# Kernel tuning notes

Hardware: AMD Instinct MI355X
Metric: run time of the kernel (lower is better)

## Reference

```python
import jax, jax.numpy as jnp
import numpy as np
from jax import lax

N_NODES = 10000
N_EDGES = 160000
F_NODE = 128
C_GCN = 64
S_SEQ = 32
T_SEQ = 96
H_LSTM = 128


def setup_inputs() -> dict:
    key = jax.random.key(0)
    ks = jax.random.split(key, 20)
    inp = {
        "sequences": jax.random.normal(ks[0], (N_NODES, T_SEQ, S_SEQ), jnp.float32),
        "edge_index": jax.random.randint(ks[1], (2, N_EDGES), 0, N_NODES, jnp.int64),
        "edge_attr": jax.random.uniform(ks[2], (N_EDGES, 1), jnp.float32),
        "node_features": jax.random.normal(ks[3], (N_NODES, F_NODE), jnp.float32),
        "node_indices": jax.random.randint(ks[4], (N_NODES,), 0, N_NODES, jnp.int64),
    }
    s_g = 1.0 / np.sqrt(F_NODE)
    inp["gcn_w"] = jax.random.uniform(ks[5], (F_NODE, C_GCN), jnp.float32, -s_g, s_g)
    inp["gcn_b"] = jnp.zeros((C_GCN,), jnp.float32)
    in0 = S_SEQ + C_GCN
    s_l = 1.0 / np.sqrt(H_LSTM)
    inp["w_ih0"] = jax.random.uniform(ks[6], (4 * H_LSTM, in0), jnp.float32, -s_l, s_l)
    inp["w_hh0"] = jax.random.uniform(ks[7], (4 * H_LSTM, H_LSTM), jnp.float32, -s_l, s_l)
    inp["b_ih0"] = jax.random.uniform(ks[8], (4 * H_LSTM,), jnp.float32, -s_l, s_l)
    inp["b_hh0"] = jax.random.uniform(ks[9], (4 * H_LSTM,), jnp.float32, -s_l, s_l)
    inp["w_ih1"] = jax.random.uniform(ks[10], (4 * H_LSTM, H_LSTM), jnp.float32, -s_l, s_l)
    inp["w_hh1"] = jax.random.uniform(ks[11], (4 * H_LSTM, H_LSTM), jnp.float32, -s_l, s_l)
    inp["b_ih1"] = jax.random.uniform(ks[12], (4 * H_LSTM,), jnp.float32, -s_l, s_l)
    inp["b_hh1"] = jax.random.uniform(ks[13], (4 * H_LSTM,), jnp.float32, -s_l, s_l)
    s_f = 1.0 / np.sqrt(H_LSTM)
    inp["fc_w"] = jax.random.uniform(ks[14], (1, H_LSTM), jnp.float32, -s_f, s_f)
    inp["fc_b"] = jnp.zeros((1,), jnp.float32)
    return inp


def gcn_conv(x, edge_index, w, b):
    """PyG GCNConv: out = D^{-1/2} (A + I) D^{-1/2} X W + b."""
    n = x.shape[0]
    xw = x @ w  # [N, C]
    loop = jnp.arange(n, dtype=edge_index.dtype)
    row = jnp.concatenate([edge_index[0], loop])  # source j
    col = jnp.concatenate([edge_index[1], loop])  # target i
    deg = jax.ops.segment_sum(jnp.ones_like(col, dtype=xw.dtype), col, num_segments=n)
    dinv = jnp.where(deg > 0, lax.rsqrt(deg), 0.0)
    norm = dinv[row] * dinv[col]  # [E+N]
    msg = xw[row] * norm[:, None]  # gather + scale
    out = jax.ops.segment_sum(msg, col, num_segments=n)  # scatter-add
    return out + b


def lstm_layer(x, w_ih, w_hh, b_ih, b_hh):
    """batch_first LSTM layer; torch gate order i,f,g,o. x: [N,T,I] -> [N,T,H]."""
    n, t, _ = x.shape
    h_dim = w_hh.shape[1]
    xg = jnp.einsum("nti,gi->ntg", x, w_ih) + b_ih + b_hh  # [N,T,4H]

    def step(carry, xt):
        h, c = carry
        g = xt + h @ w_hh.T
        i, f, gg, o = jnp.split(g, 4, axis=-1)
        c = jax.nn.sigmoid(f) * c + jax.nn.sigmoid(i) * jnp.tanh(gg)
        h = jax.nn.sigmoid(o) * jnp.tanh(c)
        return (h, c), h

    h0 = jnp.zeros((n, h_dim), x.dtype)
    _, hs = lax.scan(step, (h0, h0), jnp.swapaxes(xg, 0, 1))
    return jnp.swapaxes(hs, 0, 1)


def reference(sequences, edge_index, edge_attr, node_features, node_indices,
              gcn_w, gcn_b, w_ih0, w_hh0, b_ih0, b_hh0,
              w_ih1, w_hh1, b_ih1, b_hh1, fc_w, fc_b):
    # GCN over the static graph (dropout = identity in eval mode)
    gcn_out = gcn_conv(node_features, edge_index, gcn_w, gcn_b)  # [N, C]
    t = sequences.shape[1]
    gcn_rep = jnp.broadcast_to(gcn_out[:, None, :], (gcn_out.shape[0], t, gcn_out.shape[1]))
    combined = jnp.concatenate([sequences, gcn_rep], axis=-1)  # [N, T, S+C]
    h = lstm_layer(combined, w_ih0, w_hh0, b_ih0, b_hh0)
    h = lstm_layer(h, w_ih1, w_hh1, b_ih1, b_hh1)
    last = h[:, -1, :]  # [N, H]
    return last @ fc_w.T + fc_b  # [N, 1]
```

## Files before the change

### kernel.cpp

```cpp
#include <hip/hip_runtime.h>
#include <hip/hip_bf16.h>

typedef _Float16 half8 __attribute__((ext_vector_type(8)));
typedef float floatx4 __attribute__((ext_vector_type(4)));
typedef float floatx2 __attribute__((ext_vector_type(2)));

#define N_NODES 10000
#define F_NODE  128
#define C_GCN   64
#define N_EDGES 160000
#define T_SEQ   96
#define S_SEQ   32
#define HID     128
#define M_BLK   40
#define MT      3
#define SEQ_STRIDE 104
#define H_STRIDE   136
#define WAVE_STREAM 61440

__device__ __forceinline__ float fast_rcp(float x) { return __builtin_amdgcn_rcpf(x); }
__device__ __forceinline__ float sigm_f(float x) {
    return fast_rcp(1.0f + __expf(-x));
}
__device__ __forceinline__ float tanh_f(float x) {
    return 2.0f * fast_rcp(1.0f + __expf(-2.0f * x)) - 1.0f;
}

__global__ void k_gcn_xw(const float* __restrict__ nf, const float* __restrict__ w,
                         float* __restrict__ xw) {
    int tid = blockIdx.x * 256 + threadIdx.x;
    int n = tid >> 6, c = tid & 63;
    if (n >= N_NODES) return;
    float s = 0.f;
    #pragma unroll 8
    for (int k = 0; k < F_NODE; ++k) s = fmaf(nf[n * F_NODE + k], w[k * C_GCN + c], s);
    xw[n * C_GCN + c] = s;
}

__global__ void k_deg_init(float* __restrict__ deg) {
    int i = blockIdx.x * 256 + threadIdx.x;
    if (i < N_NODES) deg[i] = 1.0f;
}

__global__ void k_deg_count(const int* __restrict__ ei, float* __restrict__ deg) {
    int e = blockIdx.x * 256 + threadIdx.x;
    if (e < N_EDGES) atomicAdd(&deg[ei[N_EDGES + e]], 1.0f);
}

__global__ void k_dinv(const float* __restrict__ deg, float* __restrict__ dinv) {
    int i = blockIdx.x * 256 + threadIdx.x;
    if (i < N_NODES) dinv[i] = rsqrtf(deg[i]);
}

__global__ void k_gcn_self(const float* __restrict__ xw, const float* __restrict__ dinv,
                           const float* __restrict__ gb, float* __restrict__ gout) {
    int tid = blockIdx.x * 256 + threadIdx.x;
    int n = tid >> 6, c = tid & 63;
    if (n >= N_NODES) return;
    float di = dinv[n];
    gout[tid] = xw[tid] * di * di + gb[c];
}

__global__ void k_gcn_scatter(const int* __restrict__ ei, const float* __restrict__ xw,
                              const float* __restrict__ dinv, float* __restrict__ gout) {
    int e = blockIdx.x * 4 + (threadIdx.x >> 6);
    int c = threadIdx.x & 63;
    if (e >= N_EDGES) return;
    int r  = ei[e];
    int cl = ei[N_EDGES + e];
    float nm = dinv[r] * dinv[cl];
    atomicAdd(&gout[cl * C_GCN + c], xw[r * C_GCN + c] * nm);
}

__global__ void k_pack(const float* __restrict__ w_ih0, const float* __restrict__ w_hh0,
                       const float* __restrict__ w_ih1, const float* __restrict__ w_hh1,
                       half8* __restrict__ pP) {
    int tid = blockIdx.x * 256 + threadIdx.x;
    if (tid >= 8 * 15 * 4 * 64) return;
    int lane = tid & 63;
    int g    = (tid >> 6) & 3;
    int s    = (tid >> 8) % 15;
    int w    = tid / 3840;
    const float* src; int kt, K;
    if (s < 3)       { src = w_ih0; kt = s;      K = 96;  }
    else if (s < 7)  { src = w_hh0; kt = s - 3;  K = 128; }
    else if (s < 11) { src = w_ih1; kt = s - 7;  K = 128; }
    else             { src = w_hh1; kt = s - 11; K = 128; }
    int row = g * 128 + w * 16 + (lane & 15);
    int k0  = kt * 32 + (lane >> 4) * 8;
    half8 v;
    #pragma unroll
    for (int j = 0; j < 8; ++j) v[j] = (_Float16)src[row * K + k0 + j];
    pP[tid] = v;
}

__global__ void k_bsum(const float* __restrict__ bi0, const float* __restrict__ bh0,
                       const float* __restrict__ bi1, const float* __restrict__ bh1,
                       float* __restrict__ bs) {
    int i = blockIdx.x * 256 + threadIdx.x;
    if (i < 512)       bs[i] = bi0[i] + bh0[i];
    else if (i < 1024) bs[i] = bi1[i - 512] + bh1[i - 512];
}


__device__ __forceinline__ void async_copy16(const void* g, void* l) {
    __builtin_amdgcn_global_load_lds(
        (const __attribute__((address_space(1))) unsigned int*)g,
        (__attribute__((address_space(3))) unsigned int*)l, 16, 0, 0);
}

__device__ __forceinline__ void dma_slot(const char* __restrict__ src, int lane, _Float16* slot) {
    #pragma unroll
    for (int g = 0; g < 4; ++g)
        async_copy16((const void*)(src + g * 1024 + lane * 16), (void*)(slot + g * 512));
}

#define VMWAIT8() asm volatile("s_waitcnt vmcnt(8)" ::: "memory")

#define BARRIER_NOVM() do {                                   \
    asm volatile("s_waitcnt lgkmcnt(0)" ::: "memory");        \
    __builtin_amdgcn_s_barrier();                             \
    asm volatile("" ::: "memory");                            \
} while (0)

__device__ __forceinline__ void mfma_kt(floatx4 acc[4][MT], const _Float16* slot, int lane,
                                        const _Float16* A, int strideA, int koff,
                                        int l15, int quad) {
    half8 bg[4], a[MT];
    #pragma unroll
    for (int g = 0; g < 4; ++g) bg[g] = *(const half8*)(slot + g * 512 + lane * 8);
    #pragma unroll
    for (int mt = 0; mt < MT; ++mt)
        a[mt] = *(const half8*)(A + (mt * 16 + l15) * strideA + koff + quad * 8);
    #pragma unroll
    for (int g = 0; g < 4; ++g)
        #pragma unroll
        for (int mt = 0; mt < MT; ++mt)
            acc[g][mt] = __builtin_amdgcn_mfma_f32_16x16x32_f16(a[mt], bg[g], acc[g][mt], 0, 0, 0);
}

__device__ __forceinline__ void epilogue(floatx4 acc[4][MT],
                                         float c[MT][4], _Float16* Hnext,
                                         int quad, int ch) {
    #pragma unroll
    for (int mt = 0; mt < MT; ++mt) {
        #pragma unroll
        for (int r = 0; r < 4; ++r) {
            float gi = acc[0][mt][r];
            float gf = acc[1][mt][r];
            float gg = acc[2][mt][r];
            float go = acc[3][mt][r];
            float cn = sigm_f(gf) * c[mt][r] + sigm_f(gi) * tanh_f(gg);
            c[mt][r] = cn;
            float h = sigm_f(go) * tanh_f(cn);
            Hnext[(mt * 16 + quad * 4 + r) * H_STRIDE + ch] = (_Float16)h;
        }
    }
}

__global__ __launch_bounds__(512, 2) void k_lstm(
    const float* __restrict__ seq, const float* __restrict__ gcn,
    const char* __restrict__ pW, const float* __restrict__ bsum,
    const float* __restrict__ fcw, const float* __restrict__ fcb,
    float* __restrict__ out) {

    __shared__ __align__(16) _Float16 sSeq[48 * SEQ_STRIDE];
    __shared__ __align__(16) _Float16 sH0[2][48 * H_STRIDE];
    __shared__ __align__(16) _Float16 sH1[2][48 * H_STRIDE];
    __shared__ __align__(16) _Float16 sWa[8][2048];
    __shared__ __align__(16) _Float16 sWb[8][2048];
    __shared__ __align__(16) _Float16 sWc[8][2048];

    const int tid  = threadIdx.x;
    const int wid  = tid >> 6;
    const int lane = tid & 63;
    const int l15  = lane & 15;
    const int quad = lane >> 4;
    const int node0 = blockIdx.x * M_BLK;
    const int ch = wid * 16 + l15;

    const char* pWw = pW + wid * WAVE_STREAM;

#define DMA(S, RING)                  dma_slot(pWw + (S) * 4096, lane, &RING[wid][0])
#define USE(RING, Aptr, stride, koff) mfma_kt(acc, &RING[wid][0], lane, (Aptr), (stride), (koff), l15, quad)

    DMA(0, sWa);
    DMA(1, sWb);

    for (int i = tid; i < 48 * SEQ_STRIDE; i += 512) sSeq[i] = (_Float16)0.f;
    for (int i = tid; i < 48 * H_STRIDE; i += 512) {
        sH0[0][i] = (_Float16)0.f; sH0[1][i] = (_Float16)0.f;
        sH1[0][i] = (_Float16)0.f; sH1[1][i] = (_Float16)0.f;
    }

    float bias0[4], bias1[4];
    #pragma unroll
    for (int g = 0; g < 4; ++g) {
        bias0[g] = bsum[g * 128 + ch];
        bias1[g] = bsum[512 + g * 128 + ch];
    }

    float c0[MT][4] = {{0}}, c1[MT][4] = {{0}};

    __syncthreads();

    for (int i = tid; i < M_BLK * (C_GCN / 2); i += 512) {
        int r = i >> 5, cp = (i & 31) * 2;
        floatx2 v = *(const floatx2*)(gcn + (size_t)(node0 + r) * C_GCN + cp);
        sSeq[r * SEQ_STRIDE + S_SEQ + cp]     = (_Float16)v.x;
        sSeq[r * SEQ_STRIDE + S_SEQ + cp + 1] = (_Float16)v.y;
    }
    {
        int r = tid >> 4, cp = (tid & 15) * 2;
        if (tid < M_BLK * 16) {
            floatx2 v = *(const floatx2*)(seq + ((size_t)(node0 + r) * T_SEQ) * S_SEQ + cp);
            sSeq[r * SEQ_STRIDE + cp]     = (_Float16)v.x;
            sSeq[r * SEQ_STRIDE + cp + 1] = (_Float16)v.y;
        }
    }
    __syncthreads();

    floatx4 acc[4][MT];
    const int pr = tid >> 4, pc = (tid & 15) * 2;

    for (int t = 0; t < T_SEQ; ++t) {
        const int cur = t & 1, nxt = cur ^ 1;
        const _Float16* h0c = &sH0[cur][0];
        _Float16*       h0n = &sH0[nxt][0];
        const _Float16* h1c = &sH1[cur][0];
        _Float16*       h1n = &sH1[nxt][0];

        floatx2 pf0 = {0.f, 0.f}, pf1 = {0.f, 0.f};
        if (t + 1 < T_SEQ) {
            pf0 = *(const floatx2*)(seq + ((size_t)(node0 + pr) * T_SEQ + (t + 1)) * S_SEQ + pc);
            if (tid < 128) {
                int r1 = (512 + tid) >> 4, c1r = ((512 + tid) & 15) * 2;
                pf1 = *(const floatx2*)(seq + ((size_t)(node0 + r1) * T_SEQ + (t + 1)) * S_SEQ + c1r);
            }
        }

        #pragma unroll
        for (int g = 0; g < 4; ++g) {
            floatx4 bv = {bias0[g], bias0[g], bias0[g], bias0[g]};
            #pragma unroll
            for (int mt = 0; mt < MT; ++mt) acc[g][mt] = bv;
        }
        DMA(2, sWc);  VMWAIT8();  USE(sWa, sSeq, SEQ_STRIDE, 0);
        DMA(3, sWa);  VMWAIT8();  USE(sWb, sSeq, SEQ_STRIDE, 32);
        DMA(4, sWb);  VMWAIT8();  USE(sWc, sSeq, SEQ_STRIDE, 64);
        DMA(5, sWc);  VMWAIT8();  USE(sWa, h0c, H_STRIDE, 0);
        DMA(6, sWa);  VMWAIT8();  USE(sWb, h0c, H_STRIDE, 32);
        DMA(7, sWb);  VMWAIT8();  USE(sWc, h0c, H_STRIDE, 64);
        DMA(8, sWc);  VMWAIT8();  USE(sWa, h0c, H_STRIDE, 96);
        epilogue(acc, c0, h0n, quad, ch);
        BARRIER_NOVM();

        #pragma unroll
        for (int g = 0; g < 4; ++g) {
            floatx4 bv = {bias1[g], bias1[g], bias1[g], bias1[g]};
            #pragma unroll
            for (int mt = 0; mt < MT; ++mt) acc[g][mt] = bv;
        }
        DMA(9,  sWa); VMWAIT8();  USE(sWb, h0n, H_STRIDE, 0);
        DMA(10, sWb); VMWAIT8();  USE(sWc, h0n, H_STRIDE, 32);
        DMA(11, sWc); VMWAIT8();  USE(sWa, h0n, H_STRIDE, 64);
        DMA(12, sWa); VMWAIT8();  USE(sWb, h0n, H_STRIDE, 96);
        DMA(13, sWb); VMWAIT8();  USE(sWc, h1c, H_STRIDE, 0);
        DMA(14, sWc); VMWAIT8();  USE(sWa, h1c, H_STRIDE, 32);
        DMA(0,  sWa); VMWAIT8();  USE(sWb, h1c, H_STRIDE, 64);
        DMA(1,  sWb); VMWAIT8();  USE(sWc, h1c, H_STRIDE, 96);

        if (t + 1 < T_SEQ) {
            sSeq[pr * SEQ_STRIDE + pc]     = (_Float16)pf0.x;
            sSeq[pr * SEQ_STRIDE + pc + 1] = (_Float16)pf0.y;
            if (tid < 128) {
                int r1 = (512 + tid) >> 4, c1r = ((512 + tid) & 15) * 2;
                sSeq[r1 * SEQ_STRIDE + c1r]     = (_Float16)pf1.x;
                sSeq[r1 * SEQ_STRIDE + c1r + 1] = (_Float16)pf1.y;
            }
        }
        epilogue(acc, c1, h1n, quad, ch);
        BARRIER_NOVM();
    }

#undef DMA
#undef USE

    asm volatile("s_waitcnt vmcnt(0)" ::: "memory");

    if (tid < M_BLK) {
        const _Float16* h1 = &sH1[0][tid * H_STRIDE];
        float s = fcb[0];
        #pragma unroll 16
        for (int k = 0; k < HID; ++k) s = fmaf((float)h1[k], fcw[k], s);
        out[node0 + tid] = s;
    }
}

extern "C" void kernel_launch(void* const* d_in, const int* in_sizes, int n_in,
                              void* d_out, int out_size, void* d_ws, size_t ws_size,
                              hipStream_t stream) {
    const float* seq   = (const float*)d_in[0];
    const int*   ei    = (const int*)d_in[1];
    const float* nf    = (const float*)d_in[3];
    const float* gcn_w = (const float*)d_in[5];
    const float* gcn_b = (const float*)d_in[6];
    const float* w_ih0 = (const float*)d_in[7];
    const float* w_hh0 = (const float*)d_in[8];
    const float* b_ih0 = (const float*)d_in[9];
    const float* b_hh0 = (const float*)d_in[10];
    const float* w_ih1 = (const float*)d_in[11];
    const float* w_hh1 = (const float*)d_in[12];
    const float* b_ih1 = (const float*)d_in[13];
    const float* b_hh1 = (const float*)d_in[14];
    const float* fc_w  = (const float*)d_in[15];
    const float* fc_b  = (const float*)d_in[16];
    float* out = (float*)d_out;

    char* ws = (char*)d_ws;
    float* xw   = (float*)(ws);
    float* gout = (float*)(ws + 2621440);
    float* deg  = (float*)(ws + 5242880);
    float* dinv = (float*)(ws + 5283840);
    float* bsum = (float*)(ws + 5324800);
    char*  pP   = (char*)(ws + 5328896);

    k_gcn_xw     <<<2500,  256, 0, stream>>>(nf, gcn_w, xw);
    k_deg_init   <<<40,    256, 0, stream>>>(deg);
    k_deg_count  <<<625,   256, 0, stream>>>(ei, deg);
    k_dinv       <<<40,    256, 0, stream>>>(deg, dinv);
    k_gcn_self   <<<2500,  256, 0, stream>>>(xw, dinv, gcn_b, gout);
    k_gcn_scatter<<<40000, 256, 0, stream>>>(ei, xw, dinv, gout);

    k_pack<<<120, 256, 0, stream>>>(w_ih0, w_hh0, w_ih1, w_hh1, (half8*)pP);
    k_bsum<<<4,   256, 0, stream>>>(b_ih0, b_hh0, b_ih1, b_hh1, bsum);

    k_lstm<<<250, 512, 0, stream>>>(seq, gout, pP, bsum, fc_w, fc_b, out);
}
```

Measured before the change: 1.284 ms.

## Split LSTM layers across wave groups with a one-step wavefront pipeline

In the old kernel every wave ran layer 0 and then layer 1 in sequence, with a barrier between them. Now waves 0-3 run only layer 0 and waves 4-7 run only layer 1, and layer 1 trails by one timestep, so the two layers' work overlaps inside each step. Each wave now covers 32 gate channels instead of 16, and the weight packing and sequence prefetch are rearranged to match, with an extra drain iteration after the loop for layer 1. The aim is to remove the serialization between the layers and the idle time at the mid-step barrier. In exchange the two groups carry unequal work (14 versus 16 weight slots), each thread holds twice as many accumulators, and the timing of the H buffer double-buffering becomes more delicate.

```diff
diff --git a/kernel.cpp b/kernel.cpp
--- a/kernel.cpp
+++ b/kernel.cpp
@@ -16,7 +16,8 @@
 #define MT      3
 #define SEQ_STRIDE 104
 #define H_STRIDE   136
-#define WAVE_STREAM 61440
+#define L0_STREAM 57344
+#define L1_BASE   229376
 
 __device__ __forceinline__ float fast_rcp(float x) { return __builtin_amdgcn_rcpf(x); }
 __device__ __forceinline__ float sigm_f(float x) {
@@ -74,24 +75,33 @@
 
 __global__ void k_pack(const float* __restrict__ w_ih0, const float* __restrict__ w_hh0,
                        const float* __restrict__ w_ih1, const float* __restrict__ w_hh1,
-                       half8* __restrict__ pP) {
+                       char* __restrict__ pP) {
     int tid = blockIdx.x * 256 + threadIdx.x;
-    if (tid >= 8 * 15 * 4 * 64) return;
+    if (tid >= 120 * 256) return;
     int lane = tid & 63;
     int g    = (tid >> 6) & 3;
-    int s    = (tid >> 8) % 15;
-    int w    = tid / 3840;
-    const float* src; int kt, K;
-    if (s < 3)       { src = w_ih0; kt = s;      K = 96;  }
-    else if (s < 7)  { src = w_hh0; kt = s - 3;  K = 128; }
-    else if (s < 11) { src = w_ih1; kt = s - 7;  K = 128; }
-    else             { src = w_hh1; kt = s - 11; K = 128; }
-    int row = g * 128 + w * 16 + (lane & 15);
+    int gs   = tid >> 8;
+    int w, s, ch0, K, kt, n;
+    const float* src;
+    size_t base;
+    if (gs < 56) {
+        w = gs / 14; s = gs % 14; ch0 = w * 32;
+        base = (size_t)w * L0_STREAM;
+        if (s < 6) { src = w_ih0; kt = s >> 1;       n = s & 1;       K = 96;  }
+        else       { src = w_hh0; kt = (s - 6) >> 1; n = (s - 6) & 1; K = 128; }
+    } else {
+        int g2 = gs - 56;
+        w = g2 / 16; s = g2 % 16; ch0 = w * 32;
+        base = (size_t)L1_BASE + (size_t)w * 65536;
+        if (s < 8) { src = w_ih1; kt = s >> 1;       n = s & 1;       K = 128; }
+        else       { src = w_hh1; kt = (s - 8) >> 1; n = (s - 8) & 1; K = 128; }
+    }
+    int row = g * 128 + ch0 + n * 16 + (lane & 15);
     int k0  = kt * 32 + (lane >> 4) * 8;
     half8 v;
     #pragma unroll
     for (int j = 0; j < 8; ++j) v[j] = (_Float16)src[row * K + k0 + j];
-    pP[tid] = v;
+    *(half8*)(pP + base + (size_t)s * 4096 + g * 1024 + lane * 16) = v;
 }
 
 __global__ void k_bsum(const float* __restrict__ bi0, const float* __restrict__ bh0,
@@ -115,7 +125,7 @@
         async_copy16((const void*)(src + g * 1024 + lane * 16), (void*)(slot + g * 512));
 }
 
-#define VMWAIT8() asm volatile("s_waitcnt vmcnt(8)" ::: "memory")
+#define VMW(N) asm volatile("s_waitcnt vmcnt(" #N ")" ::: "memory")
 
 #define BARRIER_NOVM() do {                                   \
     asm volatile("s_waitcnt lgkmcnt(0)" ::: "memory");        \
@@ -123,39 +133,53 @@
     asm volatile("" ::: "memory");                            \
 } while (0)
 
-__device__ __forceinline__ void mfma_kt(floatx4 acc[4][MT], const _Float16* slot, int lane,
-                                        const _Float16* A, int strideA, int koff,
-                                        int l15, int quad) {
-    half8 bg[4], a[MT];
+#define LDB(BASE) {                                                         \
+    _Pragma("unroll")                                                       \
+    for (int g = 0; g < 4; ++g) bg[g] = *(const half8*)((BASE) + g * 512 + lane * 8); }
+
+#define MM(N) {                                                             \
+    _Pragma("unroll")                                                       \
+    for (int g = 0; g < 4; ++g)                                             \
+        _Pragma("unroll")                                                   \
+        for (int mt = 0; mt < MT; ++mt)                                     \
+            acc[g][N][mt] = __builtin_amdgcn_mfma_f32_16x16x32_f16(a[mt], bg[g], acc[g][N][mt], 0, 0, 0); }
+
+#define SLOT_N0(BASE, APTR, ASTR, KOFF) { LDB(BASE);                        \
+    _Pragma("unroll")                                                       \
+    for (int mt = 0; mt < MT; ++mt)                                         \
+        a[mt] = *(const half8*)((APTR) + (mt * 16 + l15) * (ASTR) + (KOFF) + quad * 8); \
+    MM(0); }
+#define SLOT_N1(BASE) { LDB(BASE); MM(1); }
+
+#define DMA2(S, BASE) dma_slot(pWw + (S) * 4096, lane, (BASE))
+
+#define ACCINIT() {                                                         \
+    _Pragma("unroll")                                                       \
+    for (int g = 0; g < 4; ++g)                                             \
+        _Pragma("unroll")                                                   \
+        for (int n = 0; n < 2; ++n) {                                       \
+            floatx4 bv = {bias[g][n], bias[g][n], bias[g][n], bias[g][n]};  \
+            _Pragma("unroll")                                               \
+            for (int mt = 0; mt < MT; ++mt) acc[g][n][mt] = bv;             \
+        } }
+
+__device__ __forceinline__ void epilogue2(floatx4 acc[4][2][MT], float cst[2][MT][4],
+                                          _Float16* H, int quad, int ch0, int l15) {
     #pragma unroll
-    for (int g = 0; g < 4; ++g) bg[g] = *(const half8*)(slot + g * 512 + lane * 8);
-    #pragma unroll
-    for (int mt = 0; mt < MT; ++mt)
-        a[mt] = *(const half8*)(A + (mt * 16 + l15) * strideA + koff + quad * 8);
-    #pragma unroll
-    for (int g = 0; g < 4; ++g)
+    for (int n = 0; n < 2; ++n)
         #pragma unroll
         for (int mt = 0; mt < MT; ++mt)
-            acc[g][mt] = __builtin_amdgcn_mfma_f32_16x16x32_f16(a[mt], bg[g], acc[g][mt], 0, 0, 0);
-}
-
-__device__ __forceinline__ void epilogue(floatx4 acc[4][MT],
-                                         float c[MT][4], _Float16* Hnext,
-                                         int quad, int ch) {
-    #pragma unroll
-    for (int mt = 0; mt < MT; ++mt) {
-        #pragma unroll
-        for (int r = 0; r < 4; ++r) {
-            float gi = acc[0][mt][r];
-            float gf = acc[1][mt][r];
-            float gg = acc[2][mt][r];
-            float go = acc[3][mt][r];
-            float cn = sigm_f(gf) * c[mt][r] + sigm_f(gi) * tanh_f(gg);
-            c[mt][r] = cn;
-            float h = sigm_f(go) * tanh_f(cn);
-            Hnext[(mt * 16 + quad * 4 + r) * H_STRIDE + ch] = (_Float16)h;
-        }
-    }
+            #pragma unroll
+            for (int r = 0; r < 4; ++r) {
+                float gi = acc[0][n][mt][r];
+                float gf = acc[1][n][mt][r];
+                float gg = acc[2][n][mt][r];
+                float go = acc[3][n][mt][r];
+                float cn = sigm_f(gf) * cst[n][mt][r] + sigm_f(gi) * tanh_f(gg);
+                cst[n][mt][r] = cn;
+                H[(mt * 16 + quad * 4 + r) * H_STRIDE + ch0 + n * 16 + l15] =
+                    (_Float16)(sigm_f(go) * tanh_f(cn));
+            }
 }
 
 __global__ __launch_bounds__(512, 2) void k_lstm(
@@ -177,15 +201,15 @@
     const int l15  = lane & 15;
     const int quad = lane >> 4;
     const int node0 = blockIdx.x * M_BLK;
-    const int ch = wid * 16 + l15;
-
-    const char* pWw = pW + wid * WAVE_STREAM;
-
-#define DMA(S, RING)                  dma_slot(pWw + (S) * 4096, lane, &RING[wid][0])
-#define USE(RING, Aptr, stride, koff) mfma_kt(acc, &RING[wid][0], lane, (Aptr), (stride), (koff), l15, quad)
-
-    DMA(0, sWa);
-    DMA(1, sWb);
+    const bool isL0 = (wid < 4);
+    const int ch0 = (wid & 3) * 32;
+
+    _Float16* const rb0 = &sWa[wid][0];
+    _Float16* const rb1 = &sWb[wid][0];
+    _Float16* const rb2 = &sWc[wid][0];
+
+    const char* pWw = pW + (isL0 ? (size_t)wid * L0_STREAM
+                                 : (size_t)L1_BASE + (size_t)(wid - 4) * 65536);
 
     for (int i = tid; i < 48 * SEQ_STRIDE; i += 512) sSeq[i] = (_Float16)0.f;
     for (int i = tid; i < 48 * H_STRIDE; i += 512) {
@@ -193,14 +217,17 @@
         sH1[0][i] = (_Float16)0.f; sH1[1][i] = (_Float16)0.f;
     }
 
-    float bias0[4], bias1[4];
-    #pragma unroll
-    for (int g = 0; g < 4; ++g) {
-        bias0[g] = bsum[g * 128 + ch];
-        bias1[g] = bsum[512 + g * 128 + ch];
-    }
-
-    float c0[MT][4] = {{0}}, c1[MT][4] = {{0}};
+    float bias[4][2];
+    {
+        int off = isL0 ? 0 : 512;
+        #pragma unroll
+        for (int g = 0; g < 4; ++g)
+            #pragma unroll
+            for (int n = 0; n < 2; ++n)
+                bias[g][n] = bsum[off + g * 128 + ch0 + n * 16 + l15];
+    }
+
+    float cst[2][MT][4] = {{{0}}};
 
     __syncthreads();
 
@@ -212,84 +239,126 @@
     }
     {
         int r = tid >> 4, cp = (tid & 15) * 2;
-        if (tid < M_BLK * 16) {
-            floatx2 v = *(const floatx2*)(seq + ((size_t)(node0 + r) * T_SEQ) * S_SEQ + cp);
-            sSeq[r * SEQ_STRIDE + cp]     = (_Float16)v.x;
-            sSeq[r * SEQ_STRIDE + cp + 1] = (_Float16)v.y;
+        floatx2 v = *(const floatx2*)(seq + ((size_t)(node0 + r) * T_SEQ) * S_SEQ + cp);
+        sSeq[r * SEQ_STRIDE + cp]     = (_Float16)v.x;
+        sSeq[r * SEQ_STRIDE + cp + 1] = (_Float16)v.y;
+        if (tid < 128) {
+            int r2 = (512 + tid) >> 4;
+            floatx2 w = *(const floatx2*)(seq + ((size_t)(node0 + r2) * T_SEQ) * S_SEQ + cp);
+            sSeq[r2 * SEQ_STRIDE + cp]     = (_Float16)w.x;
+            sSeq[r2 * SEQ_STRIDE + cp + 1] = (_Float16)w.y;
         }
     }
     __syncthreads();
 
-    floatx4 acc[4][MT];
-    const int pr = tid >> 4, pc = (tid & 15) * 2;
-
-    for (int t = 0; t < T_SEQ; ++t) {
-        const int cur = t & 1, nxt = cur ^ 1;
-        const _Float16* h0c = &sH0[cur][0];
-        _Float16*       h0n = &sH0[nxt][0];
-        const _Float16* h1c = &sH1[cur][0];
-        _Float16*       h1n = &sH1[nxt][0];
-
-        floatx2 pf0 = {0.f, 0.f}, pf1 = {0.f, 0.f};
-        if (t + 1 < T_SEQ) {
-            pf0 = *(const floatx2*)(seq + ((size_t)(node0 + pr) * T_SEQ + (t + 1)) * S_SEQ + pc);
-            if (tid < 128) {
-                int r1 = (512 + tid) >> 4, c1r = ((512 + tid) & 15) * 2;
-                pf1 = *(const floatx2*)(seq + ((size_t)(node0 + r1) * T_SEQ + (t + 1)) * S_SEQ + c1r);
-            }
+    const int tid2 = tid & 255;
+    const int pr0 = tid2 >> 4, pcp = (tid2 & 15) * 2;
+    floatx2 pfa = {0.f, 0.f}, pfb = {0.f, 0.f}, pfc = {0.f, 0.f};
+
+#define PF_ISSUE(T) do { if ((T) <= 95) {                                               \
+        pfa = *(const floatx2*)(seq + ((size_t)(node0 + pr0)      * T_SEQ + (T)) * S_SEQ + pcp); \
+        pfb = *(const floatx2*)(seq + ((size_t)(node0 + pr0 + 16) * T_SEQ + (T)) * S_SEQ + pcp); \
+        if (tid2 < 128)                                                                 \
+        pfc = *(const floatx2*)(seq + ((size_t)(node0 + pr0 + 32) * T_SEQ + (T)) * S_SEQ + pcp); \
+    } } while (0)
+
+#define COMMIT_SEQ() do { if (u < 95) {                                                 \
+        sSeq[pr0 * SEQ_STRIDE + pcp]            = (_Float16)pfa.x;                      \
+        sSeq[pr0 * SEQ_STRIDE + pcp + 1]        = (_Float16)pfa.y;                      \
+        sSeq[(pr0 + 16) * SEQ_STRIDE + pcp]     = (_Float16)pfb.x;                      \
+        sSeq[(pr0 + 16) * SEQ_STRIDE + pcp + 1] = (_Float16)pfb.y;                      \
+        if (tid2 < 128) {                                                               \
+            sSeq[(pr0 + 32) * SEQ_STRIDE + pcp]     = (_Float16)pfc.x;                  \
+            sSeq[(pr0 + 32) * SEQ_STRIDE + pcp + 1] = (_Float16)pfc.y;                  \
+        } } } while (0)
+
+    if (!isL0) PF_ISSUE(1);
+    DMA2(0, rb0);
+    DMA2(1, rb1);
+
+    floatx4 acc[4][2][MT];
+    half8 a[MT], bg[4];
+
+    for (int u = 0; u < 96; ++u) {
+        const int wp = u & 1, rp = wp ^ 1;
+
+        if (isL0) {
+            const _Float16* h0r = &sH0[rp][0];
+            _Float16*       h0w = &sH0[wp][0];
+            ACCINIT();
+            DMA2(2, rb2);  VMW(8); SLOT_N0(rb0, sSeq, SEQ_STRIDE, 0);
+            DMA2(3, rb0);  VMW(8); SLOT_N1(rb1);
+            DMA2(4, rb1);  VMW(8); SLOT_N0(rb2, sSeq, SEQ_STRIDE, 32);
+            DMA2(5, rb2);  VMW(8); SLOT_N1(rb0);
+            DMA2(6, rb0);  VMW(8); SLOT_N0(rb1, sSeq, SEQ_STRIDE, 64);
+            DMA2(7, rb1);  VMW(8); SLOT_N1(rb2);
+            BARRIER_NOVM();
+            DMA2(8, rb2);  VMW(8); SLOT_N0(rb0, h0r, H_STRIDE, 0);
+            DMA2(9, rb0);  VMW(8); SLOT_N1(rb1);
+            DMA2(10, rb1); VMW(8); SLOT_N0(rb2, h0r, H_STRIDE, 32);
+            DMA2(11, rb2); VMW(8); SLOT_N1(rb0);
+            DMA2(12, rb0); VMW(8); SLOT_N0(rb1, h0r, H_STRIDE, 64);
+            DMA2(13, rb1); VMW(8); SLOT_N1(rb2);
+            VMW(4); SLOT_N0(rb0, h0r, H_STRIDE, 96); DMA2(0, rb0);
+            VMW(4); SLOT_N1(rb1);                    DMA2(1, rb1);
+            epilogue2(acc, cst, h0w, quad, ch0, l15);
+            BARRIER_NOVM();
+        } else {
+            const _Float16* h0r = &sH0[rp][0];
+            const _Float16* h1r = &sH1[wp][0];
+            _Float16*       h1w = &sH1[rp][0];
+            ACCINIT();
+            DMA2(2, rb2);  VMW(4); SLOT_N0(rb0, h0r, H_STRIDE, 0);
+            DMA2(3, rb0);  VMW(8); SLOT_N1(rb1);
+            DMA2(4, rb1);  VMW(8); SLOT_N0(rb2, h0r, H_STRIDE, 32);
+            DMA2(5, rb2);  VMW(8); SLOT_N1(rb0);
+            DMA2(6, rb0);  VMW(8); SLOT_N0(rb1, h0r, H_STRIDE, 64);
+            DMA2(7, rb1);  VMW(8); SLOT_N1(rb2);
+            DMA2(8, rb2);  VMW(8); SLOT_N0(rb0, h0r, H_STRIDE, 96);
+            DMA2(9, rb0);  VMW(8); SLOT_N1(rb1);
+            BARRIER_NOVM();
+            COMMIT_SEQ();
+            DMA2(10, rb1); VMW(8); SLOT_N0(rb2, h1r, H_STRIDE, 0);
+            DMA2(11, rb2); VMW(8); SLOT_N1(rb0);
+            DMA2(12, rb0); VMW(8); SLOT_N0(rb1, h1r, H_STRIDE, 32);
+            DMA2(13, rb1); VMW(8); SLOT_N1(rb2);
+            DMA2(14, rb2); VMW(8); SLOT_N0(rb0, h1r, H_STRIDE, 64);
+            DMA2(15, rb0); VMW(8); SLOT_N1(rb1);
+            DMA2(1, rb1);  VMW(8); SLOT_N0(rb2, h1r, H_STRIDE, 96);
+            VMW(4); SLOT_N1(rb0); PF_ISSUE(u + 2); DMA2(0, rb0);
+            if (u) epilogue2(acc, cst, h1w, quad, ch0, l15);
+            BARRIER_NOVM();
         }
-
-        #pragma unroll
-        for (int g = 0; g < 4; ++g) {
-            floatx4 bv = {bias0[g], bias0[g], bias0[g], bias0[g]};
-            #pragma unroll
-            for (int mt = 0; mt < MT; ++mt) acc[g][mt] = bv;
-        }
-        DMA(2, sWc);  VMWAIT8();  USE(sWa, sSeq, SEQ_STRIDE, 0);
-        DMA(3, sWa);  VMWAIT8();  USE(sWb, sSeq, SEQ_STRIDE, 32);
-        DMA(4, sWb);  VMWAIT8();  USE(sWc, sSeq, SEQ_STRIDE, 64);
-        DMA(5, sWc);  VMWAIT8();  USE(sWa, h0c, H_STRIDE, 0);
-        DMA(6, sWa);  VMWAIT8();  USE(sWb, h0c, H_STRIDE, 32);
-        DMA(7, sWb);  VMWAIT8();  USE(sWc, h0c, H_STRIDE, 64);
-        DMA(8, sWc);  VMWAIT8();  USE(sWa, h0c, H_STRIDE, 96);
-        epilogue(acc, c0, h0n, quad, ch);
-        BARRIER_NOVM();
-
-        #pragma unroll
-        for (int g = 0; g < 4; ++g) {
-            floatx4 bv = {bias1[g], bias1[g], bias1[g], bias1[g]};
-            #pragma unroll
-            for (int mt = 0; mt < MT; ++mt) acc[g][mt] = bv;
-        }
-        DMA(9,  sWa); VMWAIT8();  USE(sWb, h0n, H_STRIDE, 0);
-        DMA(10, sWb); VMWAIT8();  USE(sWc, h0n, H_STRIDE, 32);
-        DMA(11, sWc); VMWAIT8();  USE(sWa, h0n, H_STRIDE, 64);
-        DMA(12, sWa); VMWAIT8();  USE(sWb, h0n, H_STRIDE, 96);
-        DMA(13, sWb); VMWAIT8();  USE(sWc, h1c, H_STRIDE, 0);
-        DMA(14, sWc); VMWAIT8();  USE(sWa, h1c, H_STRIDE, 32);
-        DMA(0,  sWa); VMWAIT8();  USE(sWb, h1c, H_STRIDE, 64);
-        DMA(1,  sWb); VMWAIT8();  USE(sWc, h1c, H_STRIDE, 96);
-
-        if (t + 1 < T_SEQ) {
-            sSeq[pr * SEQ_STRIDE + pc]     = (_Float16)pf0.x;
-            sSeq[pr * SEQ_STRIDE + pc + 1] = (_Float16)pf0.y;
-            if (tid < 128) {
-                int r1 = (512 + tid) >> 4, c1r = ((512 + tid) & 15) * 2;
-                sSeq[r1 * SEQ_STRIDE + c1r]     = (_Float16)pf1.x;
-                sSeq[r1 * SEQ_STRIDE + c1r + 1] = (_Float16)pf1.y;
-            }
-        }
-        epilogue(acc, c1, h1n, quad, ch);
-        BARRIER_NOVM();
-    }
-
-#undef DMA
-#undef USE
-
+    }
+
+    if (!isL0) {
+        const _Float16* h0r = &sH0[1][0];
+        const _Float16* h1r = &sH1[0][0];
+        _Float16*       h1w = &sH1[1][0];
+        ACCINIT();
+        DMA2(2, rb2);  VMW(4); SLOT_N0(rb0, h0r, H_STRIDE, 0);
+        DMA2(3, rb0);  VMW(8); SLOT_N1(rb1);
+        DMA2(4, rb1);  VMW(8); SLOT_N0(rb2, h0r, H_STRIDE, 32);
+        DMA2(5, rb2);  VMW(8); SLOT_N1(rb0);
+        DMA2(6, rb0);  VMW(8); SLOT_N0(rb1, h0r, H_STRIDE, 64);
+        DMA2(7, rb1);  VMW(8); SLOT_N1(rb2);
+        DMA2(8, rb2);  VMW(8); SLOT_N0(rb0, h0r, H_STRIDE, 96);
+        DMA2(9, rb0);  VMW(8); SLOT_N1(rb1);
+        DMA2(10, rb1); VMW(8); SLOT_N0(rb2, h1r, H_STRIDE, 0);
+        DMA2(11, rb2); VMW(8); SLOT_N1(rb0);
+        DMA2(12, rb0); VMW(8); SLOT_N0(rb1, h1r, H_STRIDE, 32);
+        DMA2(13, rb1); VMW(8); SLOT_N1(rb2);
+        DMA2(14, rb2); VMW(8); SLOT_N0(rb0, h1r, H_STRIDE, 64);
+        DMA2(15, rb0); VMW(8); SLOT_N1(rb1);
+        VMW(4); SLOT_N0(rb2, h1r, H_STRIDE, 96);
+        VMW(0); SLOT_N1(rb0);
+        epilogue2(acc, cst, h1w, quad, ch0, l15);
+    }
     asm volatile("s_waitcnt vmcnt(0)" ::: "memory");
+    __syncthreads();
 
     if (tid < M_BLK) {
-        const _Float16* h1 = &sH1[0][tid * H_STRIDE];
+        const _Float16* h1 = &sH1[1][tid * H_STRIDE];
         float s = fcb[0];
         #pragma unroll 16
         for (int k = 0; k < HID; ++k) s = fmaf((float)h1[k], fcw[k], s);
@@ -332,7 +401,7 @@
     k_gcn_self   <<<2500,  256, 0, stream>>>(xw, dinv, gcn_b, gout);
     k_gcn_scatter<<<40000, 256, 0, stream>>>(ei, xw, dinv, gout);
 
-    k_pack<<<120, 256, 0, stream>>>(w_ih0, w_hh0, w_ih1, w_hh1, (half8*)pP);
+    k_pack<<<120, 256, 0, stream>>>(w_ih0, w_hh0, w_ih1, w_hh1, pP);
     k_bsum<<<4,   256, 0, stream>>>(b_ih0, b_hh0, b_ih1, b_hh1, bsum);
 
     k_lstm<<<250, 512, 0, stream>>>(seq, gout, pP, bsum, fc_w, fc_b, out);
```

New measurement: 2.609 ms. 103% more time.

## Software-pipeline LDS operand reads one k-tile ahead of MFMAs in LSTM loop

Applied to the files above, without the earlier changes.

Replaces the per-k-tile load-then-MFMA helper with double-buffered register fragments (aX/aY, bX/bY), so the LDS reads for the next k-tile are issued before the MFMAs of the current one. The vmcnt wait is tightened to match the new three-slot prefetch distance. The sequence prefetch loads become unconditional, using a clamped timestep and a fixed row mapping, which removes branches. This raises register pressure and depends on the hand-written wait counts being right for the async weight DMA ring.

```diff
diff --git a/kernel.cpp b/kernel.cpp
--- a/kernel.cpp
+++ b/kernel.cpp
@@ -115,7 +115,7 @@
         async_copy16((const void*)(src + g * 1024 + lane * 16), (void*)(slot + g * 512));
 }
 
-#define VMWAIT8() asm volatile("s_waitcnt vmcnt(8)" ::: "memory")
+#define VMW(N) asm volatile("s_waitcnt vmcnt(" #N ")" ::: "memory")
 
 #define BARRIER_NOVM() do {                                   \
     asm volatile("s_waitcnt lgkmcnt(0)" ::: "memory");        \
@@ -123,21 +123,29 @@
     asm volatile("" ::: "memory");                            \
 } while (0)
 
-__device__ __forceinline__ void mfma_kt(floatx4 acc[4][MT], const _Float16* slot, int lane,
-                                        const _Float16* A, int strideA, int koff,
-                                        int l15, int quad) {
-    half8 bg[4], a[MT];
-    #pragma unroll
-    for (int g = 0; g < 4; ++g) bg[g] = *(const half8*)(slot + g * 512 + lane * 8);
-    #pragma unroll
-    for (int mt = 0; mt < MT; ++mt)
-        a[mt] = *(const half8*)(A + (mt * 16 + l15) * strideA + koff + quad * 8);
-    #pragma unroll
-    for (int g = 0; g < 4; ++g)
-        #pragma unroll
-        for (int mt = 0; mt < MT; ++mt)
-            acc[g][mt] = __builtin_amdgcn_mfma_f32_16x16x32_f16(a[mt], bg[g], acc[g][mt], 0, 0, 0);
-}
+#define RDB(BG, BUF) {                                                      \
+    _Pragma("unroll")                                                       \
+    for (int g = 0; g < 4; ++g) (BG)[g] = *(const half8*)((BUF) + g * 512 + lane * 8); }
+
+#define RDA(AA, APTR, KOFF, ASTR) {                                         \
+    _Pragma("unroll")                                                       \
+    for (int mt = 0; mt < MT; ++mt)                                         \
+        (AA)[mt] = *(const half8*)((APTR) + (mt * 16 + l15) * (ASTR) + (KOFF) + quad * 8); }
+
+#define MM(AA, BG) {                                                        \
+    _Pragma("unroll")                                                       \
+    for (int g = 0; g < 4; ++g)                                             \
+        _Pragma("unroll")                                                   \
+        for (int mt = 0; mt < MT; ++mt)                                     \
+            acc[g][mt] = __builtin_amdgcn_mfma_f32_16x16x32_f16((AA)[mt], (BG)[g], acc[g][mt], 0, 0, 0); }
+
+#define ACCINIT(B) {                                                        \
+    _Pragma("unroll")                                                       \
+    for (int g = 0; g < 4; ++g) {                                           \
+        floatx4 bv = {(B)[g], (B)[g], (B)[g], (B)[g]};                      \
+        _Pragma("unroll")                                                   \
+        for (int mt = 0; mt < MT; ++mt) acc[g][mt] = bv;                    \
+    } }
 
 __device__ __forceinline__ void epilogue(floatx4 acc[4][MT],
                                          float c[MT][4], _Float16* Hnext,
@@ -179,13 +187,16 @@
     const int node0 = blockIdx.x * M_BLK;
     const int ch = wid * 16 + l15;
 
+    _Float16* const rb0 = &sWa[wid][0];
+    _Float16* const rb1 = &sWb[wid][0];
+    _Float16* const rb2 = &sWc[wid][0];
+
     const char* pWw = pW + wid * WAVE_STREAM;
 
-#define DMA(S, RING)                  dma_slot(pWw + (S) * 4096, lane, &RING[wid][0])
-#define USE(RING, Aptr, stride, koff) mfma_kt(acc, &RING[wid][0], lane, (Aptr), (stride), (koff), l15, quad)
-
-    DMA(0, sWa);
-    DMA(1, sWb);
+#define DMA(S, RB) dma_slot(pWw + (S) * 4096, lane, (RB))
+
+    DMA(0, rb0);
+    DMA(1, rb1);
 
     for (int i = tid; i < 48 * SEQ_STRIDE; i += 512) sSeq[i] = (_Float16)0.f;
     for (int i = tid; i < 48 * H_STRIDE; i += 512) {
@@ -221,7 +232,13 @@
     __syncthreads();
 
     floatx4 acc[4][MT];
+    half8 aX[MT], aY[MT], bX[4], bY[4];
+
+    RDB(bX, rb0);
+
     const int pr = tid >> 4, pc = (tid & 15) * 2;
+    const int r1 = 32 + ((tid & 127) >> 4);
+    floatx2 pfa, pfb;
 
     for (int t = 0; t < T_SEQ; ++t) {
         const int cur = t & 1, nxt = cur ^ 1;
@@ -230,53 +247,41 @@
         const _Float16* h1c = &sH1[cur][0];
         _Float16*       h1n = &sH1[nxt][0];
 
-        floatx2 pf0 = {0.f, 0.f}, pf1 = {0.f, 0.f};
-        if (t + 1 < T_SEQ) {
-            pf0 = *(const floatx2*)(seq + ((size_t)(node0 + pr) * T_SEQ + (t + 1)) * S_SEQ + pc);
-            if (tid < 128) {
-                int r1 = (512 + tid) >> 4, c1r = ((512 + tid) & 15) * 2;
-                pf1 = *(const floatx2*)(seq + ((size_t)(node0 + r1) * T_SEQ + (t + 1)) * S_SEQ + c1r);
-            }
+        {
+            int tp = (t + 1 < T_SEQ) ? (t + 1) : (T_SEQ - 1);
+            pfa = *(const floatx2*)(seq + ((size_t)(node0 + pr) * T_SEQ + tp) * S_SEQ + pc);
+            pfb = *(const floatx2*)(seq + ((size_t)(node0 + r1) * T_SEQ + tp) * S_SEQ + pc);
         }
 
-        #pragma unroll
-        for (int g = 0; g < 4; ++g) {
-            floatx4 bv = {bias0[g], bias0[g], bias0[g], bias0[g]};
-            #pragma unroll
-            for (int mt = 0; mt < MT; ++mt) acc[g][mt] = bv;
-        }
-        DMA(2, sWc);  VMWAIT8();  USE(sWa, sSeq, SEQ_STRIDE, 0);
-        DMA(3, sWa);  VMWAIT8();  USE(sWb, sSeq, SEQ_STRIDE, 32);
-        DMA(4, sWb);  VMWAIT8();  USE(sWc, sSeq, SEQ_STRIDE, 64);
-        DMA(5, sWc);  VMWAIT8();  USE(sWa, h0c, H_STRIDE, 0);
-        DMA(6, sWa);  VMWAIT8();  USE(sWb, h0c, H_STRIDE, 32);
-        DMA(7, sWb);  VMWAIT8();  USE(sWc, h0c, H_STRIDE, 64);
-        DMA(8, sWc);  VMWAIT8();  USE(sWa, h0c, H_STRIDE, 96);
+        ACCINIT(bias0);
+        RDA(aX, sSeq, 0, SEQ_STRIDE);
+        DMA(2, rb2);  VMW(6); RDB(bY, rb1); RDA(aY, sSeq, 32, SEQ_STRIDE); MM(aX, bX);
+        DMA(3, rb0);  VMW(4); RDB(bX, rb2); RDA(aX, sSeq, 64, SEQ_STRIDE); MM(aY, bY);
+        DMA(4, rb1);  VMW(4); RDB(bY, rb0); RDA(aY, h0c, 0,  H_STRIDE);    MM(aX, bX);
+        DMA(5, rb2);  VMW(4); RDB(bX, rb1); RDA(aX, h0c, 32, H_STRIDE);    MM(aY, bY);
+        DMA(6, rb0);  VMW(4); RDB(bY, rb2); RDA(aY, h0c, 64, H_STRIDE);    MM(aX, bX);
+        DMA(7, rb1);  VMW(4); RDB(bX, rb0); RDA(aX, h0c, 96, H_STRIDE);    MM(aY, bY);
+        DMA(8, rb2);  VMW(4); RDB(bY, rb1);                                MM(aX, bX);
         epilogue(acc, c0, h0n, quad, ch);
         BARRIER_NOVM();
 
-        #pragma unroll
-        for (int g = 0; g < 4; ++g) {
-            floatx4 bv = {bias1[g], bias1[g], bias1[g], bias1[g]};
-            #pragma unroll
-            for (int mt = 0; mt < MT; ++mt) acc[g][mt] = bv;
-        }
-        DMA(9,  sWa); VMWAIT8();  USE(sWb, h0n, H_STRIDE, 0);
-        DMA(10, sWb); VMWAIT8();  USE(sWc, h0n, H_STRIDE, 32);
-        DMA(11, sWc); VMWAIT8();  USE(sWa, h0n, H_STRIDE, 64);
-        DMA(12, sWa); VMWAIT8();  USE(sWb, h0n, H_STRIDE, 96);
-        DMA(13, sWb); VMWAIT8();  USE(sWc, h1c, H_STRIDE, 0);
-        DMA(14, sWc); VMWAIT8();  USE(sWa, h1c, H_STRIDE, 32);
-        DMA(0,  sWa); VMWAIT8();  USE(sWb, h1c, H_STRIDE, 64);
-        DMA(1,  sWb); VMWAIT8();  USE(sWc, h1c, H_STRIDE, 96);
+        ACCINIT(bias1);
+        RDA(aY, h0n, 0, H_STRIDE);
+        DMA(9,  rb0); VMW(4); RDB(bX, rb2); RDA(aX, h0n, 32, H_STRIDE); MM(aY, bY);
+        DMA(10, rb1); VMW(4); RDB(bY, rb0); RDA(aY, h0n, 64, H_STRIDE); MM(aX, bX);
+        DMA(11, rb2); VMW(4); RDB(bX, rb1); RDA(aX, h0n, 96, H_STRIDE); MM(aY, bY);
+        DMA(12, rb0); VMW(4); RDB(bY, rb2); RDA(aY, h1c, 0,  H_STRIDE); MM(aX, bX);
+        DMA(13, rb1); VMW(4); RDB(bX, rb0); RDA(aX, h1c, 32, H_STRIDE); MM(aY, bY);
+        DMA(14, rb2); VMW(4); RDB(bY, rb1); RDA(aY, h1c, 64, H_STRIDE); MM(aX, bX);
+        DMA(0,  rb0); VMW(4); RDB(bX, rb2); RDA(aX, h1c, 96, H_STRIDE); MM(aY, bY);
+        DMA(1,  rb1); VMW(4); MM(aX, bX);   RDB(bX, rb0);
 
         if (t + 1 < T_SEQ) {
-            sSeq[pr * SEQ_STRIDE + pc]     = (_Float16)pf0.x;
-            sSeq[pr * SEQ_STRIDE + pc + 1] = (_Float16)pf0.y;
+            sSeq[pr * SEQ_STRIDE + pc]     = (_Float16)pfa.x;
+            sSeq[pr * SEQ_STRIDE + pc + 1] = (_Float16)pfa.y;
             if (tid < 128) {
-                int r1 = (512 + tid) >> 4, c1r = ((512 + tid) & 15) * 2;
-                sSeq[r1 * SEQ_STRIDE + c1r]     = (_Float16)pf1.x;
-                sSeq[r1 * SEQ_STRIDE + c1r + 1] = (_Float16)pf1.y;
+                sSeq[r1 * SEQ_STRIDE + pc]     = (_Float16)pfb.x;
+                sSeq[r1 * SEQ_STRIDE + pc + 1] = (_Float16)pfb.y;
             }
         }
         epilogue(acc, c1, h1n, quad, ch);
@@ -284,7 +289,6 @@
     }
 
 #undef DMA
-#undef USE
 
     asm volatile("s_waitcnt vmcnt(0)" ::: "memory");
 
```

Measured after the change: 1.250 ms. 2.7% less time.
